# Optimization experiments

Hardware: AMD Instinct MI355X
Metric: run time of the kernel (lower is better)

Reference implementation:

```python
import jax, jax.numpy as jnp
import numpy as np

B, S, E = 8, 2048, 256
NQ = 10
FF = 1024


def _cnot(state, c, t, n):
    # state: [T, 2^n]; wire 0 is the most-significant bit.
    T = state.shape[0]
    s = state.reshape((T,) + (2,) * n)
    ctrl0 = jnp.take(s, 0, axis=c + 1)
    ctrl1 = jnp.take(s, 1, axis=c + 1)
    # target axis index after removing the control axis
    t_ax = t + 1 if (t + 1) < (c + 1) else t
    ctrl1 = jnp.flip(ctrl1, axis=t_ax)  # X on target where control==1
    s = jnp.stack([ctrl0, ctrl1], axis=c + 1)
    return s.reshape(T, -1)


def _quantum_layer(tok, theta, n):
    # tok: [T, E] real; uses first n features as RX angles. Returns [T, n] PauliZ expvals.
    T = tok.shape[0]
    half = tok[:, :n] * 0.5
    c = jnp.cos(half).astype(jnp.complex64)
    s = (-1j * jnp.sin(half)).astype(jnp.complex64)
    # RX(theta)|0> = cos(t/2)|0> - i sin(t/2)|1>; build product state wire-by-wire
    state = jnp.ones((T, 1), dtype=jnp.complex64)
    for w in range(n):
        qb = jnp.stack([c[:, w], s[:, w]], axis=1)  # [T, 2]
        state = (state[:, :, None] * qb[:, None, :]).reshape(T, -1)
    # trainable RY per wire
    th = theta * 0.5
    for w in range(n):
        ct, st = jnp.cos(th[w]), jnp.sin(th[w])
        U = jnp.stack([jnp.stack([ct, -st]), jnp.stack([st, ct])]).astype(jnp.complex64)
        sr = state.reshape(T, 2 ** w, 2, -1)
        state = jnp.einsum('ij,tajb->taib', U, sr).reshape(T, -1)
    # CNOT ring
    for cw in range(n - 1):
        state = _cnot(state, cw, cw + 1, n)
    state = _cnot(state, n - 1, 0, n)
    probs = state.real ** 2 + state.imag ** 2  # [T, 2^n]
    idx = jnp.arange(2 ** n)
    bits = (idx[None, :] >> (n - 1 - jnp.arange(n)[:, None])) & 1  # [n, 2^n]
    z = (1.0 - 2.0 * bits).astype(probs.dtype)
    return probs @ z.T  # [T, n]


def setup_inputs() -> dict:
    key = jax.random.key(0)
    ks = jax.random.split(key, 6)
    return {
        'x': jax.random.normal(ks[0], (B, S, E), dtype=jnp.float32),
        'theta': jax.random.normal(ks[1], (NQ,), dtype=jnp.float32),
        'w1': jax.random.normal(ks[2], (FF, NQ), dtype=jnp.float32) * (1.0 / np.sqrt(NQ)),
        'b1': jax.random.normal(ks[3], (FF,), dtype=jnp.float32) * 0.02,
        'w2': jax.random.normal(ks[4], (E, FF), dtype=jnp.float32) * (1.0 / np.sqrt(FF)),
        'b2': jax.random.normal(ks[5], (E,), dtype=jnp.float32) * 0.02,
    }


def reference(x, theta, w1, b1, w2, b2):
    b, s, e = x.shape
    n = theta.shape[0]
    q = _quantum_layer(x.reshape(b * s, e), theta, n).reshape(b, s, n)
    # dropout is identity in eval mode
    h = jax.nn.relu(q @ w1.T + b1)
    return h @ w2.T + b2
```

## Files before the change

### kernel.cpp

```cpp
#include <hip/hip_runtime.h>
#include <hip/hip_bf16.h>
#include <math.h>

typedef __attribute__((ext_vector_type(8))) short bf16x8;
typedef __attribute__((ext_vector_type(4))) float f32x4;

#define T_TOT 16384
#define E_ 256
#define FF_ 1024
#define NQ 10
#define TB 64
#define CH 128
#define NCHUNK (FF_ / CH)
#define HGRAN (TB * CH)
#define BPAIR (32 * 512)

__device__ __forceinline__ unsigned pkbf(float a, float b) {
    __hip_bfloat162 t = __float22bfloat162_rn(make_float2(a, b));
    return *(unsigned*)&t;
}

__global__ __launch_bounds__(256) void ffq_prep(
    const float* __restrict__ w2, const float* __restrict__ w1,
    uint4* __restrict__ w2f, uint4* __restrict__ w1f)
{
    int id = blockIdx.x * 256 + threadIdx.x;
    if (id < 32768) {
        int n  = id >> 7;
        int k0 = (id & 127) * 8;
        const float4* s = (const float4*)(w2 + (size_t)n * FF_ + k0);
        float4 a = s[0], b = s[1];
        uint4 v;
        v.x = pkbf(a.x, a.y);
        v.y = pkbf(a.z, a.w);
        v.z = pkbf(b.x, b.y);
        v.w = pkbf(b.z, b.w);
        int idx = ((k0 >> 5) * 16 + (n >> 4)) * 64 + ((k0 >> 3) & 3) * 16 + (n & 15);
        w2f[idx] = v;
    } else if (id < 32768 + 4096) {
        int id2 = id - 32768;
        int l = id2 & 63, nt = id2 >> 6;
        int n = nt * 16 + (l & 15);
        int g = l >> 4;
        float o[8];
#pragma unroll
        for (int j = 0; j < 8; ++j) {
            int k = g * 8 + j;
            o[j] = (k < NQ) ? w1[n * NQ + k] : 0.f;
        }
        uint4 v;
        v.x = pkbf(o[0], o[1]);
        v.y = pkbf(o[2], o[3]);
        v.z = pkbf(o[4], o[5]);
        v.w = pkbf(o[6], o[7]);
        w1f[id2] = v;
    }
}

__global__ __launch_bounds__(512, 2) void ffq_mfma(
    const float* __restrict__ x, const float* __restrict__ theta,
    const float* __restrict__ b1, const float* __restrict__ b2,
    const bf16x8* __restrict__ w1f, const bf16x8* __restrict__ w2f,
    float* __restrict__ out)
{
    __shared__ unsigned short q_s[4 * 64 * 8];
    __shared__ unsigned short hs[2 * HGRAN];
    __shared__ unsigned short Bl[2 * BPAIR];

    const int tid = threadIdx.x;
    const int l   = tid & 63;
    const int wv  = tid >> 6;
    const int lr  = l & 15;
    const int g   = l >> 4;
    const int tb  = blockIdx.x * TB;
    const int nc0 = wv * 2;
    const int nc1 = wv * 2 + 1;

    if (tid < TB) {
        const int t = tb + tid;
        float xv[NQ];
        {
            float4 a = *(const float4*)(x + (size_t)t * E_);
            float4 b = *(const float4*)(x + (size_t)t * E_ + 4);
            float2 c = *(const float2*)(x + (size_t)t * E_ + 8);
            xv[0]=a.x; xv[1]=a.y; xv[2]=a.z; xv[3]=a.w;
            xv[4]=b.x; xv[5]=b.y; xv[6]=b.z; xv[7]=b.w;
            xv[8]=c.x; xv[9]=c.y;
        }
        float mm[NQ];
#pragma unroll
        for (int w = 0; w < NQ; ++w) mm[w] = cosf(theta[w]) * cosf(xv[w]);
        float qv[NQ];
        {
            float p = mm[0];
#pragma unroll
            for (int w = 1; w < NQ; ++w) { p *= mm[w]; qv[w] = p; }
            float p0 = mm[1];
#pragma unroll
            for (int w = 2; w < NQ; ++w) p0 *= mm[w];
            qv[0] = p0;
        }
        uint4 s0, s1;
        s0.x = pkbf(qv[0], qv[1]);
        s0.y = pkbf(qv[2], qv[3]);
        s0.z = pkbf(qv[4], qv[5]);
        s0.w = pkbf(qv[6], qv[7]);
        s1.x = pkbf(qv[8], qv[9]);
        s1.y = 0; s1.z = 0; s1.w = 0;
        int tt = tid >> 4, r = tid & 15;
        uint4* base = (uint4*)q_s + tt * 64;
        base[r]      = s0;
        base[16 + r] = s1;
        base[32 + r] = make_uint4(0, 0, 0, 0);
        base[48 + r] = make_uint4(0, 0, 0, 0);
    }

    f32x4 acc[4][2];
#pragma unroll
    for (int tt = 0; tt < 4; ++tt)
#pragma unroll
        for (int nn = 0; nn < 2; ++nn) acc[tt][nn] = (f32x4){0.f,0.f,0.f,0.f};

#define H_PHASE(cc, hdst)                                                      \
    {                                                                          \
        const int ntg = (cc) * 8 + wv;                                         \
        bf16x8 wf  = w1f[ntg * 64 + l];                                        \
        f32x4  bbc = *(const f32x4*)(b1 + ntg * 16 + g * 4);                   \
        bf16x8 qfr[4];                                                         \
        _Pragma("unroll")                                                      \
        for (int tt = 0; tt < 4; ++tt)                                         \
            qfr[tt] = ((const bf16x8*)q_s)[tt * 64 + l];                       \
        const int fl  = wv * 16 + g * 4;                 \
        const int kkl = fl >> 5;                                               \
        const int sl  = (fl & 31) >> 3;                                        \
        const int sub = (fl & 7) * 2;                                          \
        _Pragma("unroll")                                                      \
        for (int tt = 0; tt < 4; ++tt) {                                       \
            f32x4 d = __builtin_amdgcn_mfma_f32_16x16x32_bf16(                 \
                    wf, qfr[tt], bbc, 0, 0, 0);                                \
            unsigned p0 = pkbf(fmaxf(d[0], 0.f), fmaxf(d[1], 0.f));            \
            unsigned p1 = pkbf(fmaxf(d[2], 0.f), fmaxf(d[3], 0.f));            \
            unsigned byteoff = (unsigned)((tt * 4 + kkl) * 64 + lr + 16 * sl)  \
                               * 16u + (unsigned)sub;                          \
            *(uint2*)((char*)(hdst) + byteoff) = make_uint2(p0, p1);           \
        }                                                                      \
    }

    bf16x8 stg[4];
#pragma unroll
    for (int r = 0; r < 4; ++r)
        stg[r] = w2f[(0 * 32 + r * 8 + wv) * 64 + l];
#pragma unroll
    for (int r = 0; r < 4; ++r)
        ((bf16x8*)Bl)[(r * 8 + wv) * 64 + l] = stg[r];
    __syncthreads();

    H_PHASE(0, hs)
#pragma unroll
    for (int r = 0; r < 4; ++r)
        stg[r] = w2f[(1 * 32 + r * 8 + wv) * 64 + l];
    __syncthreads();

#pragma unroll 2
    for (int p = 0; p < 16; ++p) {
        const bf16x8* bcur = (const bf16x8*)(Bl + (p & 1) * BPAIR);
        bf16x8*       bnxt = (bf16x8*)(Bl + ((p & 1) ^ 1) * BPAIR);
        const bf16x8* hc   = (const bf16x8*)(hs + ((p >> 1) & 1) * HGRAN);

#pragma unroll
        for (int e = 0; e < 2; ++e) {
            const int kkl = ((p & 1) << 1) + e;
            bf16x8 af[4];
#pragma unroll
            for (int tt = 0; tt < 4; ++tt)
                af[tt] = hc[(tt * 4 + kkl) * 64 + l];
            bf16x8 b0 = bcur[(e * 16 + nc0) * 64 + l];
            bf16x8 b1v = bcur[(e * 16 + nc1) * 64 + l];
#pragma unroll
            for (int tt = 0; tt < 4; ++tt)
                acc[tt][0] = __builtin_amdgcn_mfma_f32_16x16x32_bf16(
                    af[tt], b0, acc[tt][0], 0, 0, 0);
#pragma unroll
            for (int tt = 0; tt < 4; ++tt)
                acc[tt][1] = __builtin_amdgcn_mfma_f32_16x16x32_bf16(
                    af[tt], b1v, acc[tt][1], 0, 0, 0);
        }

        if ((p & 1) == 1 && p < 15) {
            H_PHASE((p >> 1) + 1, hs + (((p >> 1) & 1) ^ 1) * HGRAN)
        }

        if (p < 15) {
#pragma unroll
            for (int r = 0; r < 4; ++r)
                bnxt[(r * 8 + wv) * 64 + l] = stg[r];
            if (p < 14) {
#pragma unroll
                for (int r = 0; r < 4; ++r)
                    stg[r] = w2f[((p + 2) * 32 + r * 8 + wv) * 64 + l];
            }
        }
        __syncthreads();
    }
#undef H_PHASE

    {
        const int col0 = nc0 * 16 + lr;
        const int col1 = col0 + 16;
        const float bb0 = b2[col0];
        const float bb1 = b2[col1];
#pragma unroll
        for (int tt = 0; tt < 4; ++tt) {
#pragma unroll
            for (int r = 0; r < 4; ++r) {
                int tr = tb + tt * 16 + g * 4 + r;
                out[(size_t)tr * E_ + col0] = acc[tt][0][r] + bb0;
                out[(size_t)tr * E_ + col1] = acc[tt][1][r] + bb1;
            }
        }
    }
}

extern "C" void kernel_launch(void* const* d_in, const int* in_sizes, int n_in,
                              void* d_out, int out_size, void* d_ws, size_t ws_size,
                              hipStream_t stream) {
    const float* x     = (const float*)d_in[0];
    const float* theta = (const float*)d_in[1];
    const float* w1    = (const float*)d_in[2];
    const float* b1    = (const float*)d_in[3];
    const float* w2    = (const float*)d_in[4];
    const float* b2    = (const float*)d_in[5];
    float* out = (float*)d_out;

    uint4* w2f = (uint4*)d_ws;
    uint4* w1f = (uint4*)((char*)d_ws + 512 * 1024);

    hipLaunchKernelGGL(ffq_prep, dim3(144), dim3(256), 0, stream,
                       w2, w1, w2f, w1f);
    hipLaunchKernelGGL(ffq_mfma, dim3(T_TOT / TB), dim3(512), 0, stream,
                       x, theta, b1, b2,
                       (const bf16x8*)w1f, (const bf16x8*)w2f, out);
}
```

Before: 27.65 us.

## Give each wave an independent token-column tile and drop block barriers

Restructures the MFMA kernel so each wave owns a 64-token by 32-column output tile, computes the quantum features and full hidden layer itself into a private LDS slice, and streams W2 fragments directly from global memory with register prefetch. This removes per-step __syncthreads and shared W2 staging. It trades them for the hidden layer being recomputed by every column-wave (8x redundant first-layer MFMAs and cosines) and more L2 reads of W2. It also adds s_setprio around the second-layer MFMAs.

```diff
diff --git a/kernel.cpp b/kernel.cpp
--- a/kernel.cpp
+++ b/kernel.cpp
@@ -9,11 +9,9 @@
 #define E_ 256
 #define FF_ 1024
 #define NQ 10
-#define TB 64
 #define CH 128
 #define NCHUNK (FF_ / CH)
-#define HGRAN (TB * CH)
-#define BPAIR (32 * 512)
+#define HG (64 * CH)
 
 __device__ __forceinline__ unsigned pkbf(float a, float b) {
     __hip_bfloat162 t = __float22bfloat162_rn(make_float2(a, b));
@@ -57,27 +55,34 @@
     }
 }
 
-__global__ __launch_bounds__(512, 2) void ffq_mfma(
+__global__ __launch_bounds__(256, 2) void ffq_mfma(
     const float* __restrict__ x, const float* __restrict__ theta,
     const float* __restrict__ b1, const float* __restrict__ b2,
     const bf16x8* __restrict__ w1f, const bf16x8* __restrict__ w2f,
     float* __restrict__ out)
 {
-    __shared__ unsigned short q_s[4 * 64 * 8];
-    __shared__ unsigned short hs[2 * HGRAN];
-    __shared__ unsigned short Bl[2 * BPAIR];
-
-    const int tid = threadIdx.x;
-    const int l   = tid & 63;
-    const int wv  = tid >> 6;
-    const int lr  = l & 15;
-    const int g   = l >> 4;
-    const int tb  = blockIdx.x * TB;
-    const int nc0 = wv * 2;
-    const int nc1 = wv * 2 + 1;
-
-    if (tid < TB) {
-        const int t = tb + tid;
+    __shared__ unsigned short hs[4 * HG];
+
+    const int tid  = threadIdx.x;
+    const int l    = tid & 63;
+    const int wv   = tid >> 6;
+    const int lr   = l & 15;
+    const int g    = l >> 4;
+    const int wid  = blockIdx.x * 4 + wv;
+    const int tb   = (wid >> 3) * 64;
+    const int nc0  = (wid & 7) * 2;
+    const int nc1  = nc0 + 1;
+
+    unsigned short* hsw = hs + wv * HG;
+
+    float ct[NQ];
+#pragma unroll
+    for (int w = 0; w < NQ; ++w) ct[w] = cosf(theta[w]);
+
+    bf16x8 qf[4];
+#pragma unroll
+    for (int tt = 0; tt < 4; ++tt) {
+        const int t = tb + tt * 16 + lr;
         float xv[NQ];
         {
             float4 a = *(const float4*)(x + (size_t)t * E_);
@@ -87,10 +92,9 @@
             xv[4]=b.x; xv[5]=b.y; xv[6]=b.z; xv[7]=b.w;
             xv[8]=c.x; xv[9]=c.y;
         }
-        float mm[NQ];
-#pragma unroll
-        for (int w = 0; w < NQ; ++w) mm[w] = cosf(theta[w]) * cosf(xv[w]);
-        float qv[NQ];
+        float mm[NQ], qv[NQ];
+#pragma unroll
+        for (int w = 0; w < NQ; ++w) mm[w] = ct[w] * cosf(xv[w]);
         {
             float p = mm[0];
 #pragma unroll
@@ -100,19 +104,15 @@
             for (int w = 2; w < NQ; ++w) p0 *= mm[w];
             qv[0] = p0;
         }
-        uint4 s0, s1;
-        s0.x = pkbf(qv[0], qv[1]);
-        s0.y = pkbf(qv[2], qv[3]);
-        s0.z = pkbf(qv[4], qv[5]);
-        s0.w = pkbf(qv[6], qv[7]);
-        s1.x = pkbf(qv[8], qv[9]);
-        s1.y = 0; s1.z = 0; s1.w = 0;
-        int tt = tid >> 4, r = tid & 15;
-        uint4* base = (uint4*)q_s + tt * 64;
-        base[r]      = s0;
-        base[16 + r] = s1;
-        base[32 + r] = make_uint4(0, 0, 0, 0);
-        base[48 + r] = make_uint4(0, 0, 0, 0);
+        uint4 v;
+#pragma unroll
+        for (int h2 = 0; h2 < 4; ++h2) {
+            int k0 = g * 8 + h2 * 2;
+            float a0 = (k0     < NQ) ? qv[k0]     : 0.f;
+            float a1 = (k0 + 1 < NQ) ? qv[k0 + 1] : 0.f;
+            ((unsigned*)&v)[h2] = pkbf(a0, a1);
+        }
+        qf[tt] = __builtin_bit_cast(bf16x8, v);
     }
 
     f32x4 acc[4][2];
@@ -121,101 +121,68 @@
 #pragma unroll
         for (int nn = 0; nn < 2; ++nn) acc[tt][nn] = (f32x4){0.f,0.f,0.f,0.f};
 
-#define H_PHASE(cc, hdst)                                                      \
-    {                                                                          \
-        const int ntg = (cc) * 8 + wv;                                         \
-        bf16x8 wf  = w1f[ntg * 64 + l];                                        \
-        f32x4  bbc = *(const f32x4*)(b1 + ntg * 16 + g * 4);                   \
-        bf16x8 qfr[4];                                                         \
-        _Pragma("unroll")                                                      \
-        for (int tt = 0; tt < 4; ++tt)                                         \
-            qfr[tt] = ((const bf16x8*)q_s)[tt * 64 + l];                       \
-        const int fl  = wv * 16 + g * 4;                 \
-        const int kkl = fl >> 5;                                               \
-        const int sl  = (fl & 31) >> 3;                                        \
-        const int sub = (fl & 7) * 2;                                          \
-        _Pragma("unroll")                                                      \
-        for (int tt = 0; tt < 4; ++tt) {                                       \
-            f32x4 d = __builtin_amdgcn_mfma_f32_16x16x32_bf16(                 \
-                    wf, qfr[tt], bbc, 0, 0, 0);                                \
-            unsigned p0 = pkbf(fmaxf(d[0], 0.f), fmaxf(d[1], 0.f));            \
-            unsigned p1 = pkbf(fmaxf(d[2], 0.f), fmaxf(d[3], 0.f));            \
-            unsigned byteoff = (unsigned)((tt * 4 + kkl) * 64 + lr + 16 * sl)  \
-                               * 16u + (unsigned)sub;                          \
-            *(uint2*)((char*)(hdst) + byteoff) = make_uint2(p0, p1);           \
-        }                                                                      \
-    }
-
-    bf16x8 stg[4];
-#pragma unroll
-    for (int r = 0; r < 4; ++r)
-        stg[r] = w2f[(0 * 32 + r * 8 + wv) * 64 + l];
-#pragma unroll
-    for (int r = 0; r < 4; ++r)
-        ((bf16x8*)Bl)[(r * 8 + wv) * 64 + l] = stg[r];
-    __syncthreads();
-
-    H_PHASE(0, hs)
-#pragma unroll
-    for (int r = 0; r < 4; ++r)
-        stg[r] = w2f[(1 * 32 + r * 8 + wv) * 64 + l];
-    __syncthreads();
-
-#pragma unroll 2
-    for (int p = 0; p < 16; ++p) {
-        const bf16x8* bcur = (const bf16x8*)(Bl + (p & 1) * BPAIR);
-        bf16x8*       bnxt = (bf16x8*)(Bl + ((p & 1) ^ 1) * BPAIR);
-        const bf16x8* hc   = (const bf16x8*)(hs + ((p >> 1) & 1) * HGRAN);
-
-#pragma unroll
-        for (int e = 0; e < 2; ++e) {
-            const int kkl = ((p & 1) << 1) + e;
+    bf16x8 bc0 = w2f[(0 * 16 + nc0) * 64 + l];
+    bf16x8 bc1 = w2f[(0 * 16 + nc1) * 64 + l];
+    bf16x8 wfc = w1f[0 * 64 + l];
+
+    for (int c = 0; c < NCHUNK; ++c) {
+#pragma unroll
+        for (int nt = 0; nt < 8; ++nt) {
+            const int ntg = c * 8 + nt;
+            bf16x8 wfn = (ntg + 1 < 64) ? w1f[(ntg + 1) * 64 + l] : wfc;
+            f32x4  bbc = *(const f32x4*)(b1 + ntg * 16 + g * 4);
+            const int fl  = nt * 16 + g * 4;
+            const int kkl = fl >> 5;
+            const int sl  = (fl & 31) >> 3;
+            const int sub = (fl & 7) * 2;
+#pragma unroll
+            for (int tt = 0; tt < 4; ++tt) {
+                f32x4 d = __builtin_amdgcn_mfma_f32_16x16x32_bf16(
+                        wfc, qf[tt], bbc, 0, 0, 0);
+                unsigned p0 = pkbf(fmaxf(d[0], 0.f), fmaxf(d[1], 0.f));
+                unsigned p1 = pkbf(fmaxf(d[2], 0.f), fmaxf(d[3], 0.f));
+                unsigned byteoff = (unsigned)((tt * 4 + kkl) * 64 + lr
+                                   + 16 * sl) * 16u + (unsigned)sub;
+                *(uint2*)((char*)hsw + byteoff) = make_uint2(p0, p1);
+            }
+            wfc = wfn;
+        }
+
+        const bf16x8* hc = (const bf16x8*)hsw;
+#pragma unroll
+        for (int kkl = 0; kkl < 4; ++kkl) {
+            const int kk  = c * 4 + kkl;
+            const int kkn = (kk + 1 < 32) ? kk + 1 : 31;
+            bf16x8 bn0 = w2f[(kkn * 16 + nc0) * 64 + l];
+            bf16x8 bn1 = w2f[(kkn * 16 + nc1) * 64 + l];
             bf16x8 af[4];
 #pragma unroll
             for (int tt = 0; tt < 4; ++tt)
                 af[tt] = hc[(tt * 4 + kkl) * 64 + l];
-            bf16x8 b0 = bcur[(e * 16 + nc0) * 64 + l];
-            bf16x8 b1v = bcur[(e * 16 + nc1) * 64 + l];
+            __builtin_amdgcn_s_setprio(1);
 #pragma unroll
             for (int tt = 0; tt < 4; ++tt)
                 acc[tt][0] = __builtin_amdgcn_mfma_f32_16x16x32_bf16(
-                    af[tt], b0, acc[tt][0], 0, 0, 0);
+                    af[tt], bc0, acc[tt][0], 0, 0, 0);
 #pragma unroll
             for (int tt = 0; tt < 4; ++tt)
                 acc[tt][1] = __builtin_amdgcn_mfma_f32_16x16x32_bf16(
-                    af[tt], b1v, acc[tt][1], 0, 0, 0);
-        }
-
-        if ((p & 1) == 1 && p < 15) {
-            H_PHASE((p >> 1) + 1, hs + (((p >> 1) & 1) ^ 1) * HGRAN)
-        }
-
-        if (p < 15) {
-#pragma unroll
-            for (int r = 0; r < 4; ++r)
-                bnxt[(r * 8 + wv) * 64 + l] = stg[r];
-            if (p < 14) {
-#pragma unroll
-                for (int r = 0; r < 4; ++r)
-                    stg[r] = w2f[((p + 2) * 32 + r * 8 + wv) * 64 + l];
-            }
-        }
-        __syncthreads();
-    }
-#undef H_PHASE
-
-    {
-        const int col0 = nc0 * 16 + lr;
-        const int col1 = col0 + 16;
-        const float bb0 = b2[col0];
-        const float bb1 = b2[col1];
+                    af[tt], bc1, acc[tt][1], 0, 0, 0);
+            __builtin_amdgcn_s_setprio(0);
+            bc0 = bn0; bc1 = bn1;
+        }
+    }
+
+#pragma unroll
+    for (int nn = 0; nn < 2; ++nn) {
+        const int col = (nc0 + nn) * 16 + lr;
+        const float bbv = b2[col];
 #pragma unroll
         for (int tt = 0; tt < 4; ++tt) {
 #pragma unroll
             for (int r = 0; r < 4; ++r) {
                 int tr = tb + tt * 16 + g * 4 + r;
-                out[(size_t)tr * E_ + col0] = acc[tt][0][r] + bb0;
-                out[(size_t)tr * E_ + col1] = acc[tt][1][r] + bb1;
+                out[(size_t)tr * E_ + col] = acc[tt][nn][r] + bbv;
             }
         }
     }
@@ -237,7 +204,7 @@
 
     hipLaunchKernelGGL(ffq_prep, dim3(144), dim3(256), 0, stream,
                        w2, w1, w2f, w1f);
-    hipLaunchKernelGGL(ffq_mfma, dim3(T_TOT / TB), dim3(512), 0, stream,
+    hipLaunchKernelGGL(ffq_mfma, dim3(512), dim3(256), 0, stream,
                        x, theta, b1, b2,
                        (const bf16x8*)w1f, (const bf16x8*)w2f, out);
 }
```

Measured after the change: 44.04 us. +59.3%, slower.
